# Kernel tuning notes

Hardware: AMD Instinct MI355X
Metric: run time of the kernel (lower is better)

## Reference

```python
import jax, jax.numpy as jnp
import numpy as np

B, N, F_IN, H, FO = 4, 2048, 256, 4, 64


def setup_inputs() -> dict:
    key = jax.random.key(0)
    k1, k2, k3, k4, k5 = jax.random.split(key, 5)
    x = jax.random.normal(k1, (B, N, F_IN), dtype=jnp.float32)
    # random 0/1 adjacency with self-loops so every row of softmax is finite
    adj = jax.random.randint(k2, (N, N), 0, 2).astype(jnp.float32)
    adj = jnp.maximum(adj, jnp.eye(N, dtype=jnp.float32))
    # parameters (xavier-uniform style)
    lim_w = float(np.sqrt(6.0 / (F_IN + H * FO)))
    W = jax.random.uniform(k3, (F_IN, H * FO), minval=-lim_w, maxval=lim_w, dtype=jnp.float32)
    lim_a = float(np.sqrt(6.0 / (H + FO)))
    a_src = jax.random.uniform(k4, (H, FO), minval=-lim_a, maxval=lim_a, dtype=jnp.float32)
    a_dst = jax.random.uniform(k5, (H, FO), minval=-lim_a, maxval=lim_a, dtype=jnp.float32)
    return {"x": x, "adj": adj, "W": W, "a_src": a_src, "a_dst": a_dst}


def reference(x, adj, W, a_src, a_dst):
    # h: (B, N, H, FO)
    h = (x @ W).reshape(B, N, H, FO)
    attn_src = jnp.einsum("bnhf,hf->bnh", h, a_src)  # (B,N,H)
    attn_dst = jnp.einsum("bnhf,hf->bnh", h, a_dst)  # (B,N,H)
    # scores[b,i,j,h] = src[b,i,h] + dst[b,j,h]
    scores = attn_src[:, :, None, :] + attn_dst[:, None, :, :]
    scores = jax.nn.leaky_relu(scores, negative_slope=0.2)
    mask = (adj == 0)[None, :, :, None]  # (1,N,N,1)
    scores = jnp.where(mask, -jnp.inf, scores)
    attn = jax.nn.softmax(scores, axis=2)  # softmax over neighbors j
    # dropout is identity in eval mode / p=0
    out = jnp.einsum("bijh,bjhf->bihf", attn, h)  # (B,N,H,FO)
    return out.reshape(B, N, H * FO)  # concat=True
```

## Files before the change

kernel.cpp:

```cpp
#include <hip/hip_runtime.h>
#include <hip/hip_bf16.h>
#include <math.h>

#define B 4
#define N 2048
#define FIN 256
#define H 4
#define FO 64
#define M (B*N)
#define HF (H*FO)

typedef __attribute__((ext_vector_type(8))) short short8;
typedef __attribute__((ext_vector_type(8))) _Float16 half8;
typedef __attribute__((ext_vector_type(2))) _Float16 half2v;
typedef __attribute__((ext_vector_type(4))) float float4v;
typedef __attribute__((ext_vector_type(4))) int int4v;

#if __has_builtin(__builtin_amdgcn_exp2f)
#define EXP2(x) __builtin_amdgcn_exp2f(x)
#else
#define EXP2(x) exp2f(x)
#endif

static __device__ __forceinline__ void split_pair(float x0, float x1,
                                                  unsigned int& hi, unsigned int& lo) {
  unsigned int u0 = __builtin_bit_cast(unsigned int, x0);
  unsigned int u1 = __builtin_bit_cast(unsigned int, x1);
  hi = (u0 >> 16) | (u1 & 0xffff0000u);
  float h0 = __builtin_bit_cast(float, u0 & 0xffff0000u);
  float h1 = __builtin_bit_cast(float, u1 & 0xffff0000u);
  unsigned int l0 = __builtin_bit_cast(unsigned int, x0 - h0);
  unsigned int l1 = __builtin_bit_cast(unsigned int, x1 - h1);
  lo = (l0 >> 16) | (l1 & 0xffff0000u);
}

static __device__ __forceinline__ unsigned int fenc(float f) {
  unsigned int b = __builtin_bit_cast(unsigned int, f);
  return (b & 0x80000000u) ? ~b : (b | 0x80000000u);
}
static __device__ __forceinline__ float fdec(unsigned int e) {
  unsigned int b = (e & 0x80000000u) ? (e & 0x7fffffffu) : ~e;
  return __builtin_bit_cast(float, b);
}

static __device__ __forceinline__ unsigned int f16pk(float a, float b) {
  auto h = __builtin_amdgcn_cvt_pkrtz(a, b);
  return __builtin_bit_cast(unsigned int, h);
}

struct Chunk {
  short8 b0, b1, b2, b3;
  uint4 e1, e2;
  uint4 m0, m1;
};

__global__ __launch_bounds__(256) void prep_wx(const float* __restrict__ Wsrc,
                                               const float* __restrict__ X,
                                               unsigned short* __restrict__ Wf_hi,
                                               unsigned short* __restrict__ Wf_lo,
                                               unsigned short* __restrict__ Xf_hi,
                                               unsigned short* __restrict__ Xf_lo,
                                               unsigned int* __restrict__ DmaxEnc) {
  const int blk = blockIdx.x;
  const int t = threadIdx.x;
  __shared__ float lds[64][65];
  if (blk < 16) {
    if (blk == 0 && t < 16) DmaxEnc[t] = 0u;
    const int k0 = (blk >> 2) * 64;
    const int h  = blk & 3;
    const int n0 = h * 64;
    const int c4 = (t & 15) * 4;
    #pragma unroll
    for (int rep = 0; rep < 4; ++rep) {
      const int kl = (t >> 4) + 16 * rep;
      const float4 v = *(const float4*)(Wsrc + (size_t)(k0 + kl) * HF + n0 + c4);
      lds[kl][c4 + 0] = v.x; lds[kl][c4 + 1] = v.y;
      lds[kl][c4 + 2] = v.z; lds[kl][c4 + 3] = v.w;
    }
    __syncthreads();
    #pragma unroll
    for (int rep = 0; rep < 2; ++rep) {
      const int s   = t + rep * 256;
      const int kcl = s >> 8;
      const int tt  = (s >> 6) & 3;
      const int ln  = s & 63;
      const int fL  = tt * 16 + (ln & 15);
      const int kb  = kcl * 32 + (ln >> 4) * 8;
      unsigned int hv[4], lv[4];
      #pragma unroll
      for (int p = 0; p < 4; ++p)
        split_pair(lds[kb + 2 * p][fL], lds[kb + 2 * p + 1][fL], hv[p], lv[p]);
      const size_t off = ((((size_t)h * 8 + (k0 >> 5) + kcl) * 4 + tt) << 9) + ln * 8;
      *(uint4*)(Wf_hi + off) = make_uint4(hv[0], hv[1], hv[2], hv[3]);
      *(uint4*)(Wf_lo + off) = make_uint4(lv[0], lv[1], lv[2], lv[3]);
    }
    return;
  }
  const int xb2   = blk - 16;
  const int xblk  = xb2 >> 2;
  const int ktile = xb2 & 3;
  const int mrow0 = xblk * 64;
  const int k0 = ktile * 64;
  const int c4 = (t & 15) * 4;
  #pragma unroll
  for (int rep = 0; rep < 4; ++rep) {
    const int rl = (t >> 4) + 16 * rep;
    const float4 v = *(const float4*)(X + (size_t)(mrow0 + rl) * FIN + k0 + c4);
    lds[rl][c4 + 0] = v.x; lds[rl][c4 + 1] = v.y;
    lds[rl][c4 + 2] = v.z; lds[rl][c4 + 3] = v.w;
  }
  __syncthreads();
  #pragma unroll
  for (int rep = 0; rep < 2; ++rep) {
    const int s   = t + rep * 256;
    const int mt  = s >> 7;
    const int kcl = (s >> 6) & 1;
    const int ln  = s & 63;
    const int mrl = mt * 16 + (ln & 15);
    const int kb  = kcl * 32 + (ln >> 4) * 8;
    unsigned int hv[4], lv[4];
    #pragma unroll
    for (int p = 0; p < 4; ++p)
      split_pair(lds[mrl][kb + 2 * p], lds[mrl][kb + 2 * p + 1], hv[p], lv[p]);
    const size_t off = (((size_t)(xblk * 4 + mt) * 8 + (ktile * 2 + kcl)) << 9) + ln * 8;
    *(uint4*)(Xf_hi + off) = make_uint4(hv[0], hv[1], hv[2], hv[3]);
    *(uint4*)(Xf_lo + off) = make_uint4(lv[0], lv[1], lv[2], lv[3]);
  }
}

__global__ __launch_bounds__(256) void gemm_fused(const unsigned short* __restrict__ Xf_hi,
                                                  const unsigned short* __restrict__ Xf_lo,
                                                  const unsigned short* __restrict__ Wf_hi,
                                                  const unsigned short* __restrict__ Wf_lo,
                                                  const float* __restrict__ adj,
                                                  const float* __restrict__ a_src,
                                                  const float* __restrict__ a_dst,
                                                  float* __restrict__ Srcv,
                                                  unsigned short* __restrict__ E1h,
                                                  unsigned short* __restrict__ E2h,
                                                  unsigned int* __restrict__ DmaxEnc,
                                                  unsigned short* __restrict__ msk,
                                                  unsigned short* __restrict__ Hf) {
  if (blockIdx.x >= 512) {
    const int row = blockIdx.x - 512;
    const int t = threadIdx.x;
    const float* ar = adj + (size_t)row * N + t * 8;
    const float4 v0 = *(const float4*)(ar);
    const float4 v1 = *(const float4*)(ar + 4);
    const unsigned int d0 = (v0.x != 0.f ? 0x0000FFFFu : 0u) | (v0.y != 0.f ? 0xFFFF0000u : 0u);
    const unsigned int d1 = (v0.z != 0.f ? 0x0000FFFFu : 0u) | (v0.w != 0.f ? 0xFFFF0000u : 0u);
    const unsigned int d2 = (v1.x != 0.f ? 0x0000FFFFu : 0u) | (v1.y != 0.f ? 0xFFFF0000u : 0u);
    const unsigned int d3 = (v1.z != 0.f ? 0x0000FFFFu : 0u) | (v1.w != 0.f ? 0xFFFF0000u : 0u);
    *(uint4*)(msk + (size_t)row * N + t * 8) = make_uint4(d0, d1, d2, d3);
    return;
  }
  __shared__ unsigned short sh[64][72];
  __shared__ float smax[4];
  const int xcd  = blockIdx.x & 7;
  const int slot = blockIdx.x >> 3;
  const int mb = xcd * 16 + (slot >> 2);
  const int h  = slot & 3;
  const int w = threadIdx.x >> 6, lane = threadIdx.x & 63;
  const int fl = lane & 15, quad = lane >> 4;
  const float L2E = 1.4426950408889634f;

  const float4v zero = {0.f, 0.f, 0.f, 0.f};
  float4v acc[4] = {zero, zero, zero, zero};

  const size_t abase = (((size_t)(mb * 4 + w) * 8) << 9) + lane * 8;
  #pragma unroll
  for (int kc = 0; kc < 8; ++kc) {
    const short8 Ahi = *(const short8*)(Xf_hi + abase + ((size_t)kc << 9));
    const short8 Alo = *(const short8*)(Xf_lo + abase + ((size_t)kc << 9));
    #pragma unroll
    for (int t = 0; t < 4; ++t) {
      const size_t woff = ((((size_t)h * 8 + kc) * 4 + t) << 9) + lane * 8;
      const short8 Bhi = *(const short8*)(Wf_hi + woff);
      const short8 Blo = *(const short8*)(Wf_lo + woff);
      acc[t] = __builtin_amdgcn_mfma_f32_16x16x32_bf16(Ahi, Bhi, acc[t], 0, 0, 0);
      acc[t] = __builtin_amdgcn_mfma_f32_16x16x32_bf16(Alo, Bhi, acc[t], 0, 0, 0);
      acc[t] = __builtin_amdgcn_mfma_f32_16x16x32_bf16(Ahi, Blo, acc[t], 0, 0, 0);
    }
  }

  const int bb  = (mb * 64) >> 11;
  const int n0w = (mb * 64) & (N - 1);
  const int bh  = bb * H + h;
  float as[4], ad[4];
  #pragma unroll
  for (int t = 0; t < 4; ++t) {
    as[t] = a_src[h * FO + t * 16 + fl];
    ad[t] = a_dst[h * FO + t * 16 + fl];
  }
  float wmax = -INFINITY;
  #pragma unroll
  for (int reg = 0; reg < 4; ++reg) {
    float sv = 0.f, dv = 0.f;
    #pragma unroll
    for (int t = 0; t < 4; ++t) {
      sv = fmaf(acc[t][reg], as[t], sv);
      dv = fmaf(acc[t][reg], ad[t], dv);
    }
    #pragma unroll
    for (int off = 1; off <= 8; off <<= 1) {
      sv += __shfl_xor(sv, off, 64);
      dv += __shfl_xor(dv, off, 64);
    }
    wmax = fmaxf(wmax, dv);
    if (fl == 0) {
      const int node = n0w + w * 16 + quad * 4 + reg;
      Srcv[(bh << 11) + node] = sv;
      const unsigned int eu = f16pk(EXP2(dv * L2E),
                                    EXP2(dv * (0.2f * L2E)));
      E1h[(bh << 11) + node] = (unsigned short)(eu & 0xffffu);
      E2h[(bh << 11) + node] = (unsigned short)(eu >> 16);
    }
  }
  wmax = fmaxf(wmax, __shfl_xor(wmax, 16, 64));
  wmax = fmaxf(wmax, __shfl_xor(wmax, 32, 64));
  if (lane == 0) smax[w] = wmax;

  #pragma unroll
  for (int t = 0; t < 4; ++t) {
    const int nl = w * 16 + quad * 4;
    *(unsigned int*)&sh[t * 16 + fl][nl]     = f16pk(acc[t][0], acc[t][1]);
    *(unsigned int*)&sh[t * 16 + fl][nl + 2] = f16pk(acc[t][2], acc[t][3]);
  }
  __syncthreads();
  if (threadIdx.x == 0) {
    const float bmax = fmaxf(fmaxf(smax[0], smax[1]), fmaxf(smax[2], smax[3]));
    atomicMax(DmaxEnc + bh, fenc(bmax));
  }
  const int jc0 = n0w >> 5;
  #pragma unroll
  for (int rep = 0; rep < 2; ++rep) {
    const int s = (int)threadIdx.x + rep * 256;
    const int jcl = s >> 8;
    const int tt  = (s >> 6) & 3;
    const int ln  = s & 63;
    const int f    = tt * 16 + (ln & 15);
    const int node = jcl * 32 + (ln >> 4) * 8;
    unsigned short* dsth = Hf + (((size_t)bh * 64 + jc0 + jcl) * 4 + tt) * 512 + ln * 8;
    *(uint4*)dsth = *(const uint4*)&sh[f][node];
  }
}

__global__ __launch_bounds__(512) void gat_mfma(const unsigned short* __restrict__ msk,
                                                const float* __restrict__ Src,
                                                const unsigned short* __restrict__ E1h,
                                                const unsigned short* __restrict__ E2h,
                                                const unsigned int* __restrict__ DmaxEnc,
                                                const unsigned short* __restrict__ Hf,
                                                float* __restrict__ out) {
  const int xcd  = blockIdx.x & 7;
  const int slot = blockIdx.x >> 3;
  const int b    = xcd >> 1;
  const int i0   = ((xcd & 1) * 32 + slot) * 32;
  const int w    = threadIdx.x >> 6;
  const int lane = threadIdx.x & 63;
  const int h    = w & 3;
  const int jh   = w >> 2;
  const int bh   = b * H + h;
  const int fl   = lane & 15;
  const int kk   = (lane >> 4) * 8;
  const float L2E = 1.4426950408889634f;

  const int row0 = i0 + fl;
  const int row1 = i0 + 16 + fl;
  const float dmx = fdec(DmaxEnc[bh]);
  const float s0 = Src[(bh << 11) + row0];
  const float s1 = Src[(bh << 11) + row1];
  const float u0 = s0 + dmx, m0 = fmaxf(u0, 0.2f * u0);
  const float u1 = s1 + dmx, m1 = fmaxf(u1, 0.2f * u1);
  const float c1a = EXP2((s0 - m0) * L2E), c2a = EXP2((0.2f * s0 - m0) * L2E);
  const float c1b = EXP2((s1 - m1) * L2E), c2b = EXP2((0.2f * s1 - m1) * L2E);
  const half2v c1a2 = {(_Float16)c1a, (_Float16)c1a};
  const half2v c2a2 = {(_Float16)c2a, (_Float16)c2a};
  const half2v c1b2 = {(_Float16)c1b, (_Float16)c1b};
  const half2v c2b2 = {(_Float16)c2b, (_Float16)c2b};
  const unsigned short* mr0 = msk + (size_t)row0 * N + kk;
  const unsigned short* mr1 = msk + (size_t)row1 * N + kk;
  const unsigned short* hfb = Hf + (size_t)bh * 64 * 2048 + lane * 8;
  const unsigned short* e1b = E1h + (bh << 11);
  const unsigned short* e2b = E2h + (bh << 11);

  half8 ones;
  #pragma unroll
  for (int jj = 0; jj < 8; ++jj) ones[jj] = (_Float16)1.0f;

  const float4v zero = {0.f, 0.f, 0.f, 0.f};
  float4v acc[2][4];
  float4v accL[2];
  #pragma unroll
  for (int rt = 0; rt < 2; ++rt) {
    accL[rt] = zero;
    #pragma unroll
    for (int t = 0; t < 4; ++t) acc[rt][t] = zero;
  }

  const int jbeg = jh * (N / 2);

  auto loadc = [&](int J) -> Chunk {
    Chunk c;
    const unsigned short* hc = hfb + (size_t)(J >> 5) * 2048;
    c.b0 = *(const short8*)(hc + 0 * 512);
    c.b1 = *(const short8*)(hc + 1 * 512);
    c.b2 = *(const short8*)(hc + 2 * 512);
    c.b3 = *(const short8*)(hc + 3 * 512);
    c.e1 = *(const uint4*)(e1b + J + kk);
    c.e2 = *(const uint4*)(e2b + J + kk);
    c.m0 = *(const uint4*)(mr0 + J);
    c.m1 = *(const uint4*)(mr1 + J);
    return c;
  };

  auto compute = [&](const Chunk& c) {
    const unsigned int e1w[4] = {c.e1.x, c.e1.y, c.e1.z, c.e1.w};
    const unsigned int e2w[4] = {c.e2.x, c.e2.y, c.e2.z, c.e2.w};
    const unsigned int m0w[4] = {c.m0.x, c.m0.y, c.m0.z, c.m0.w};
    const unsigned int m1w[4] = {c.m1.x, c.m1.y, c.m1.z, c.m1.w};
    int p0i[4], p1i[4];
    #pragma unroll
    for (int p = 0; p < 4; ++p) {
      const half2v e1 = __builtin_bit_cast(half2v, e1w[p]);
      const half2v e2 = __builtin_bit_cast(half2v, e2w[p]);
      const half2v wa = __builtin_elementwise_max(c1a2 * e1, c2a2 * e2);
      const half2v wb = __builtin_elementwise_max(c1b2 * e1, c2b2 * e2);
      p0i[p] = (int)(__builtin_bit_cast(unsigned int, wa) & m0w[p]);
      p1i[p] = (int)(__builtin_bit_cast(unsigned int, wb) & m1w[p]);
    }
    const half8 p0 = __builtin_bit_cast(half8, (int4v){p0i[0], p0i[1], p0i[2], p0i[3]});
    const half8 p1 = __builtin_bit_cast(half8, (int4v){p1i[0], p1i[1], p1i[2], p1i[3]});
    const half8 hb0 = __builtin_bit_cast(half8, c.b0);
    const half8 hb1 = __builtin_bit_cast(half8, c.b1);
    const half8 hb2 = __builtin_bit_cast(half8, c.b2);
    const half8 hb3 = __builtin_bit_cast(half8, c.b3);
    acc[0][0] = __builtin_amdgcn_mfma_f32_16x16x32_f16(p0, hb0, acc[0][0], 0, 0, 0);
    acc[0][1] = __builtin_amdgcn_mfma_f32_16x16x32_f16(p0, hb1, acc[0][1], 0, 0, 0);
    acc[0][2] = __builtin_amdgcn_mfma_f32_16x16x32_f16(p0, hb2, acc[0][2], 0, 0, 0);
    acc[0][3] = __builtin_amdgcn_mfma_f32_16x16x32_f16(p0, hb3, acc[0][3], 0, 0, 0);
    accL[0]   = __builtin_amdgcn_mfma_f32_16x16x32_f16(p0, ones, accL[0], 0, 0, 0);
    acc[1][0] = __builtin_amdgcn_mfma_f32_16x16x32_f16(p1, hb0, acc[1][0], 0, 0, 0);
    acc[1][1] = __builtin_amdgcn_mfma_f32_16x16x32_f16(p1, hb1, acc[1][1], 0, 0, 0);
    acc[1][2] = __builtin_amdgcn_mfma_f32_16x16x32_f16(p1, hb2, acc[1][2], 0, 0, 0);
    acc[1][3] = __builtin_amdgcn_mfma_f32_16x16x32_f16(p1, hb3, acc[1][3], 0, 0, 0);
    accL[1]   = __builtin_amdgcn_mfma_f32_16x16x32_f16(p1, ones, accL[1], 0, 0, 0);
  };

  Chunk A = loadc(jbeg);
  for (int it = 0; it < 30; it += 2) {
    Chunk Bc = loadc(jbeg + (it + 1) * 32);
    compute(A);
    A = loadc(jbeg + (it + 2) * 32);
    compute(Bc);
  }
  {
    Chunk Bc = loadc(jbeg + 31 * 32);
    compute(A);
    compute(Bc);
  }

  __shared__ float4v parts[4][64][11];
  if (jh == 1) {
    #pragma unroll
    for (int rt = 0; rt < 2; ++rt) {
      #pragma unroll
      for (int t = 0; t < 4; ++t) parts[h][lane][rt * 5 + t] = acc[rt][t];
      parts[h][lane][rt * 5 + 4] = accL[rt];
    }
  }
  __syncthreads();
  if (jh == 0) {
    #pragma unroll
    for (int rt = 0; rt < 2; ++rt) {
      #pragma unroll
      for (int t = 0; t < 4; ++t) acc[rt][t] += parts[h][lane][rt * 5 + t];
      accL[rt] += parts[h][lane][rt * 5 + 4];
    }
    const int quad = lane >> 4;
    #pragma unroll
    for (int rt = 0; rt < 2; ++rt) {
      #pragma unroll
      for (int reg = 0; reg < 4; ++reg) {
        const int r = i0 + rt * 16 + quad * 4 + reg;
        const float invl = 1.f / accL[rt][reg];
        float* op = out + ((size_t)(b * N) + r) * HF + h * FO + fl;
        #pragma unroll
        for (int t = 0; t < 4; ++t) op[t * 16] = acc[rt][t][reg] * invl;
      }
    }
  }
}

extern "C" void kernel_launch(void* const* d_in, const int* in_sizes, int n_in,
                              void* d_out, int out_size, void* d_ws, size_t ws_size,
                              hipStream_t stream) {
  const float* x     = (const float*)d_in[0];
  const float* adj   = (const float*)d_in[1];
  const float* W     = (const float*)d_in[2];
  const float* a_src = (const float*)d_in[3];
  const float* a_dst = (const float*)d_in[4];
  float* out = (float*)d_out;

  char* p = (char*)d_ws;
  float* Srcv = (float*)p;                  p += (size_t)B * H * N * 4;
  unsigned short* E1h = (unsigned short*)p; p += (size_t)B * H * N * 2;
  unsigned short* E2h = (unsigned short*)p; p += (size_t)B * H * N * 2;
  unsigned int* DmaxEnc = (unsigned int*)p; p += 256;
  unsigned short* Wfh = (unsigned short*)p; p += (size_t)HF * FIN * 2;
  unsigned short* Wfl = (unsigned short*)p; p += (size_t)HF * FIN * 2;
  unsigned short* Xfh = (unsigned short*)p; p += (size_t)M * FIN * 2;
  unsigned short* Xfl = (unsigned short*)p; p += (size_t)M * FIN * 2;
  unsigned short* Hf  = (unsigned short*)p; p += (size_t)M * HF * 2;
  unsigned short* msk = (unsigned short*)p;

  prep_wx<<<dim3(528), dim3(256), 0, stream>>>(W, x, Wfh, Wfl, Xfh, Xfl, DmaxEnc);
  gemm_fused<<<dim3(512 + N), dim3(256), 0, stream>>>(Xfh, Xfl, Wfh, Wfl, adj,
                                                      a_src, a_dst,
                                                      Srcv, E1h, E2h, DmaxEnc,
                                                      msk, Hf);
  gat_mfma<<<dim3(B * (N / 32)), dim3(512), 0, stream>>>(msk,
                                                         Srcv, E1h, E2h, DmaxEnc, Hf, out);
}
```

Before: 121.6 us.

## Store adjacency mask as bytes and deepen load prefetch to four chunks

The adjacency mask is now stored as one byte per entry instead of 16-bit words. In the attention kernel the bytes are expanded back to 16-bit masks with byte-permute instructions, which halves mask traffic in both the producer and the consumer. The main loop also moves from double buffering to keeping three chunks in flight ahead of compute, so more load latency is hidden. The deeper buffering raises register pressure in a 512-thread block, which could cut occupancy or cause spills.

```diff
diff --git a/kernel.cpp b/kernel.cpp
--- a/kernel.cpp
+++ b/kernel.cpp
@@ -48,10 +48,17 @@
   return __builtin_bit_cast(unsigned int, h);
 }
 
+static __device__ __forceinline__ unsigned int expand_lo(unsigned int w) {
+  return __builtin_amdgcn_perm(0u, w, 0x01010000u);
+}
+static __device__ __forceinline__ unsigned int expand_hi(unsigned int w) {
+  return __builtin_amdgcn_perm(0u, w, 0x03030202u);
+}
+
 struct Chunk {
   short8 b0, b1, b2, b3;
   uint4 e1, e2;
-  uint4 m0, m1;
+  uint2 m0, m1;
 };
 
 __global__ __launch_bounds__(256) void prep_wx(const float* __restrict__ Wsrc,
@@ -139,7 +146,7 @@
                                                   unsigned short* __restrict__ E1h,
                                                   unsigned short* __restrict__ E2h,
                                                   unsigned int* __restrict__ DmaxEnc,
-                                                  unsigned short* __restrict__ msk,
+                                                  unsigned char* __restrict__ msk,
                                                   unsigned short* __restrict__ Hf) {
   if (blockIdx.x >= 512) {
     const int row = blockIdx.x - 512;
@@ -147,11 +154,11 @@
     const float* ar = adj + (size_t)row * N + t * 8;
     const float4 v0 = *(const float4*)(ar);
     const float4 v1 = *(const float4*)(ar + 4);
-    const unsigned int d0 = (v0.x != 0.f ? 0x0000FFFFu : 0u) | (v0.y != 0.f ? 0xFFFF0000u : 0u);
-    const unsigned int d1 = (v0.z != 0.f ? 0x0000FFFFu : 0u) | (v0.w != 0.f ? 0xFFFF0000u : 0u);
-    const unsigned int d2 = (v1.x != 0.f ? 0x0000FFFFu : 0u) | (v1.y != 0.f ? 0xFFFF0000u : 0u);
-    const unsigned int d3 = (v1.z != 0.f ? 0x0000FFFFu : 0u) | (v1.w != 0.f ? 0xFFFF0000u : 0u);
-    *(uint4*)(msk + (size_t)row * N + t * 8) = make_uint4(d0, d1, d2, d3);
+    const unsigned int d0 = (v0.x != 0.f ? 0x000000FFu : 0u) | (v0.y != 0.f ? 0x0000FF00u : 0u) |
+                            (v0.z != 0.f ? 0x00FF0000u : 0u) | (v0.w != 0.f ? 0xFF000000u : 0u);
+    const unsigned int d1 = (v1.x != 0.f ? 0x000000FFu : 0u) | (v1.y != 0.f ? 0x0000FF00u : 0u) |
+                            (v1.z != 0.f ? 0x00FF0000u : 0u) | (v1.w != 0.f ? 0xFF000000u : 0u);
+    *(uint2*)(msk + (size_t)row * N + t * 8) = make_uint2(d0, d1);
     return;
   }
   __shared__ unsigned short sh[64][72];
@@ -245,7 +252,7 @@
   }
 }
 
-__global__ __launch_bounds__(512) void gat_mfma(const unsigned short* __restrict__ msk,
+__global__ __launch_bounds__(512) void gat_mfma(const unsigned char* __restrict__ msk,
                                                 const float* __restrict__ Src,
                                                 const unsigned short* __restrict__ E1h,
                                                 const unsigned short* __restrict__ E2h,
@@ -278,8 +285,8 @@
   const half2v c2a2 = {(_Float16)c2a, (_Float16)c2a};
   const half2v c1b2 = {(_Float16)c1b, (_Float16)c1b};
   const half2v c2b2 = {(_Float16)c2b, (_Float16)c2b};
-  const unsigned short* mr0 = msk + (size_t)row0 * N + kk;
-  const unsigned short* mr1 = msk + (size_t)row1 * N + kk;
+  const unsigned char* mr0 = msk + (size_t)row0 * N + kk;
+  const unsigned char* mr1 = msk + (size_t)row1 * N + kk;
   const unsigned short* hfb = Hf + (size_t)bh * 64 * 2048 + lane * 8;
   const unsigned short* e1b = E1h + (bh << 11);
   const unsigned short* e2b = E2h + (bh << 11);
@@ -309,16 +316,18 @@
     c.b3 = *(const short8*)(hc + 3 * 512);
     c.e1 = *(const uint4*)(e1b + J + kk);
     c.e2 = *(const uint4*)(e2b + J + kk);
-    c.m0 = *(const uint4*)(mr0 + J);
-    c.m1 = *(const uint4*)(mr1 + J);
+    c.m0 = *(const uint2*)(mr0 + J);
+    c.m1 = *(const uint2*)(mr1 + J);
     return c;
   };
 
   auto compute = [&](const Chunk& c) {
     const unsigned int e1w[4] = {c.e1.x, c.e1.y, c.e1.z, c.e1.w};
     const unsigned int e2w[4] = {c.e2.x, c.e2.y, c.e2.z, c.e2.w};
-    const unsigned int m0w[4] = {c.m0.x, c.m0.y, c.m0.z, c.m0.w};
-    const unsigned int m1w[4] = {c.m1.x, c.m1.y, c.m1.z, c.m1.w};
+    const unsigned int m0w[4] = {expand_lo(c.m0.x), expand_hi(c.m0.x),
+                                 expand_lo(c.m0.y), expand_hi(c.m0.y)};
+    const unsigned int m1w[4] = {expand_lo(c.m1.x), expand_hi(c.m1.x),
+                                 expand_lo(c.m1.y), expand_hi(c.m1.y)};
     int p0i[4], p1i[4];
     #pragma unroll
     for (int p = 0; p < 4; ++p) {
@@ -347,17 +356,25 @@
     accL[1]   = __builtin_amdgcn_mfma_f32_16x16x32_f16(p1, ones, accL[1], 0, 0, 0);
   };
 
-  Chunk A = loadc(jbeg);
-  for (int it = 0; it < 30; it += 2) {
-    Chunk Bc = loadc(jbeg + (it + 1) * 32);
+  Chunk A  = loadc(jbeg + 0 * 32);
+  Chunk Bc = loadc(jbeg + 1 * 32);
+  Chunk C  = loadc(jbeg + 2 * 32);
+  for (int it = 0; it < 28; it += 4) {
+    Chunk D = loadc(jbeg + (it + 3) * 32);
     compute(A);
-    A = loadc(jbeg + (it + 2) * 32);
+    A = loadc(jbeg + (it + 4) * 32);
     compute(Bc);
+    Bc = loadc(jbeg + (it + 5) * 32);
+    compute(C);
+    C = loadc(jbeg + (it + 6) * 32);
+    compute(D);
   }
   {
-    Chunk Bc = loadc(jbeg + 31 * 32);
+    Chunk D = loadc(jbeg + 31 * 32);
     compute(A);
     compute(Bc);
+    compute(C);
+    compute(D);
   }
 
   __shared__ float4v parts[4][64][11];
@@ -412,7 +429,7 @@
   unsigned short* Xfh = (unsigned short*)p; p += (size_t)M * FIN * 2;
   unsigned short* Xfl = (unsigned short*)p; p += (size_t)M * FIN * 2;
   unsigned short* Hf  = (unsigned short*)p; p += (size_t)M * HF * 2;
-  unsigned short* msk = (unsigned short*)p;
+  unsigned char* msk = (unsigned char*)p;
 
   prep_wx<<<dim3(528), dim3(256), 0, stream>>>(W, x, Wfh, Wfl, Xfh, Xfl, DmaxEnc);
   gemm_fused<<<dim3(512 + N), dim3(256), 0, stream>>>(Xfh, Xfl, Wfh, Wfl, adj,
```

Result: no change. 122.4 us (+0.6%).
